# Kernel tuning notes

Measured on AMD Instinct MI355X. Metric: run time of the kernel, lower is better.

Reference implementation:

```python
import jax, jax.numpy as jnp
import numpy as np

BATCH, INPUT_DIM, BOND_DIM, OUTPUT_DIM = 4096, 1024, 32, 512


def setup_inputs() -> dict:
    key = jax.random.key(0)
    k1, k2, k3 = jax.random.split(key, 3)
    # inputs centered at 1 so the length-1024 chain product stays O(1) in fp32
    inputs = 1.0 + 0.05 * jax.random.normal(k1, (BATCH, INPUT_DIM), dtype=jnp.float32)
    # cores scaled ~ glorot so each [bond,bond] step roughly preserves norm
    cores = jax.random.normal(k2, (INPUT_DIM, BOND_DIM, BOND_DIM), dtype=jnp.float32) / jnp.sqrt(jnp.float32(BOND_DIM))
    projection = jax.random.normal(k3, (BOND_DIM, OUTPUT_DIM), dtype=jnp.float32) * 0.05
    bias = jnp.zeros((OUTPUT_DIM,), dtype=jnp.float32)
    return {"inputs": inputs, "cores": cores, "projection": projection, "bias": bias}


def reference(inputs, cores, projection, bias):
    # MPS chain: boundary_{i+1}[b,k] = sum_j boundary_i[b,j] * x_i[b] * core_i[j,k]
    batch = inputs.shape[0]
    bond = cores.shape[1]
    boundary0 = jnp.ones((batch, bond), dtype=inputs.dtype)

    def step(boundary, xc):
        x_i, core_i = xc  # x_i: [batch], core_i: [bond, bond]
        new_boundary = (boundary * x_i[:, None]) @ core_i  # [batch, bond]
        return new_boundary, None

    xs = (inputs.T, cores)  # scan over input_dim axis
    final_boundary, _ = jax.lax.scan(step, boundary0, xs)
    return final_boundary @ projection + bias
```

## Files before the change

kernel.cpp:

```cpp
#include <hip/hip_runtime.h>


__device__ __forceinline__ void mm32(const float* __restrict__ A,
                                     const float* __restrict__ B,
                                     float* __restrict__ C, int tid) {
    const int j = tid >> 3;
    const int kq = tid & 7;
    float a[32];
    const float4* __restrict__ A4 = (const float4*)(A + j * 32);
#pragma unroll
    for (int t = 0; t < 8; ++t) {
        float4 v = A4[t];
        a[4 * t + 0] = v.x; a[4 * t + 1] = v.y;
        a[4 * t + 2] = v.z; a[4 * t + 3] = v.w;
    }
    const float4* __restrict__ B4 = (const float4*)B;
    float4 acc = make_float4(0.f, 0.f, 0.f, 0.f);
#pragma unroll
    for (int m = 0; m < 32; ++m) {
        float4 b = B4[m * 8 + kq];
        acc.x = fmaf(a[m], b.x, acc.x);
        acc.y = fmaf(a[m], b.y, acc.y);
        acc.z = fmaf(a[m], b.z, acc.z);
        acc.w = fmaf(a[m], b.w, acc.w);
    }
    ((float4*)(C + j * 32))[kq] = acc;
}

__global__ __launch_bounds__(256) void k_seg4(const float* __restrict__ cores,
                                              float* __restrict__ l1) {
    __shared__ __align__(16) float c[4 * 1024];
    __shared__ __align__(16) float ping[1024];
    __shared__ __align__(16) float pong[1024];
    const int tid = threadIdx.x;
    const int s = blockIdx.x;
    const float4* src = (const float4*)(cores + (size_t)s * 4096);
    float4* cd = (float4*)c;
#pragma unroll
    for (int t = 0; t < 4; ++t) cd[tid + 256 * t] = src[tid + 256 * t];
    __syncthreads();
    mm32(c, c + 1024, ping, tid);
    __syncthreads();
    mm32(ping, c + 2048, pong, tid);
    __syncthreads();
    mm32(pong, c + 3072, ping, tid);
    __syncthreads();
    ((float4*)(l1 + (size_t)s * 1024))[tid] = ((const float4*)ping)[tid];
}

__global__ __launch_bounds__(256) void k_seg8(const float* __restrict__ l1,
                                              float* __restrict__ l2) {
    __shared__ __align__(16) float m[8 * 1024];
    __shared__ __align__(16) float ping[1024];
    __shared__ __align__(16) float pong[1024];
    const int tid = threadIdx.x;
    const int s = blockIdx.x;
    const float4* src = (const float4*)(l1 + (size_t)s * 8192);
    float4* md = (float4*)m;
#pragma unroll
    for (int t = 0; t < 8; ++t) md[tid + 256 * t] = src[tid + 256 * t];
    __syncthreads();
    mm32(m, m + 1024, ping, tid);
    __syncthreads();
    float* A = ping;
    float* C = pong;
    for (int t = 2; t < 8; ++t) {
        mm32(A, m + t * 1024, C, tid);
        __syncthreads();
        float* tmp = A; A = C; C = tmp;
    }
    ((float4*)(l2 + (size_t)s * 1024))[tid] = ((const float4*)A)[tid];
}

__global__ __launch_bounds__(64) void k_chain(const float* __restrict__ l2,
                                              const float* __restrict__ proj,
                                              float* __restrict__ q) {
    __shared__ __align__(16) float M[2][2048];
    __shared__ __align__(16) float sc[2][32];
    const int lane = threadIdx.x;
    const int k = lane & 31;
    const float4* src = (const float4*)l2;
    float4 pf[8];
#pragma unroll
    for (int t = 0; t < 8; ++t) pf[t] = src[lane + 64 * t];
#pragma unroll
    for (int t = 0; t < 8; ++t) ((float4*)M[0])[lane + 64 * t] = pf[t];
    __syncthreads();
    float v[32];
#pragma unroll
    for (int j = 0; j < 32; ++j) v[j] = 1.0f;
    for (int c = 0; c < 16; ++c) {
        if (c + 1 < 16) {
#pragma unroll
            for (int t = 0; t < 8; ++t)
                pf[t] = src[(c + 1) * 512 + lane + 64 * t];
        }
        const float* Mc = M[c & 1];
#pragma unroll
        for (int s = 0; s < 2; ++s) {
            const float* mat = Mc + s * 1024;
            float acc = 0.f;
#pragma unroll
            for (int j = 0; j < 32; ++j)
                acc = fmaf(v[j], mat[j * 32 + k], acc);
            const int pb = (2 * c + s) & 1;
            if (lane < 32) sc[pb][k] = acc;
            __syncthreads();
#pragma unroll
            for (int j = 0; j < 32; ++j) v[j] = sc[pb][j];
        }
        if (c + 1 < 16) {
            __syncthreads();
#pragma unroll
            for (int t = 0; t < 8; ++t)
                ((float4*)M[(c + 1) & 1])[lane + 64 * t] = pf[t];
            __syncthreads();
        }
    }
    const float4* P4 = (const float4*)proj;
    float4* q4 = (float4*)q;
#pragma unroll
    for (int h = 0; h < 2; ++h) {
        const int o4 = h * 64 + lane;
        float4 acc = make_float4(0.f, 0.f, 0.f, 0.f);
#pragma unroll
        for (int j = 0; j < 32; ++j) {
            float4 pv = P4[j * 128 + o4];
            acc.x = fmaf(v[j], pv.x, acc.x);
            acc.y = fmaf(v[j], pv.y, acc.y);
            acc.z = fmaf(v[j], pv.z, acc.z);
            acc.w = fmaf(v[j], pv.w, acc.w);
        }
        q4[o4] = acc;
    }
}

__global__ __launch_bounds__(256) void k_out(const float* __restrict__ inputs,
                                             const float* __restrict__ q,
                                             const float* __restrict__ bias,
                                             float* __restrict__ out) {
    const int lane = threadIdx.x & 63;
    const int wid = threadIdx.x >> 6;
    const int row = blockIdx.x * 4 + wid;
    const float4* in4 = (const float4*)(inputs + (size_t)row * 1024);
    float4 x0 = in4[lane];
    float4 x1 = in4[lane + 64];
    float4 x2 = in4[lane + 128];
    float4 x3 = in4[lane + 192];
    float p = ((x0.x * x0.y) * (x0.z * x0.w)) * ((x1.x * x1.y) * (x1.z * x1.w)) *
              ((x2.x * x2.y) * (x2.z * x2.w)) * ((x3.x * x3.y) * (x3.z * x3.w));
#pragma unroll
    for (int msk = 1; msk < 64; msk <<= 1) p *= __shfl_xor(p, msk);
    const float4* q4 = (const float4*)q;
    const float4* b4 = (const float4*)bias;
    float4* o4 = (float4*)(out + (size_t)row * 512);
#pragma unroll
    for (int t = 0; t < 2; ++t) {
        float4 qq = q4[lane + 64 * t];
        float4 bb = b4[lane + 64 * t];
        float4 r;
        r.x = fmaf(p, qq.x, bb.x);
        r.y = fmaf(p, qq.y, bb.y);
        r.z = fmaf(p, qq.z, bb.z);
        r.w = fmaf(p, qq.w, bb.w);
        o4[lane + 64 * t] = r;
    }
}

extern "C" void kernel_launch(void* const* d_in, const int* in_sizes, int n_in,
                              void* d_out, int out_size, void* d_ws, size_t ws_size,
                              hipStream_t stream) {
    const float* inputs = (const float*)d_in[0];
    const float* cores  = (const float*)d_in[1];
    const float* proj   = (const float*)d_in[2];
    const float* bias   = (const float*)d_in[3];
    float* out = (float*)d_out;
    float* w  = (float*)d_ws;
    float* l1 = w;
    float* l2 = w + 256 * 1024;
    float* q  = w + 256 * 1024 + 32 * 1024;

    k_seg4<<<256, 256, 0, stream>>>(cores, l1);
    k_seg8<<<32, 256, 0, stream>>>(l1, l2);
    k_chain<<<1, 64, 0, stream>>>(l2, proj, q);
    k_out<<<1024, 256, 0, stream>>>(inputs, q, bias, out);
}
```

Measured before the change: 101.0 us.

## Fuse row-product into core-segment kernel and rebalance chain reduction tree levels

Per-row input products are now computed in the first kernel, which loads the input rows while the 4-core segment products run, so the output kernel only reads a precomputed scalar. The second-level reduction now combines 16 segments per block (16 blocks) instead of 8, and the serial chain kernel handles 16 matrices using wave shuffles instead of LDS and barriers. The output kernel stages q and bias in LDS and writes 8 rows per block. The deeper second level does more serial matmuls per block with fewer blocks, trading parallelism for a shorter single-block serial tail.

```diff
diff --git a/kernel.cpp b/kernel.cpp
--- a/kernel.cpp
+++ b/kernel.cpp
@@ -27,17 +27,32 @@
     ((float4*)(C + j * 32))[kq] = acc;
 }
 
-__global__ __launch_bounds__(256) void k_seg4(const float* __restrict__ cores,
-                                              float* __restrict__ l1) {
+__global__ __launch_bounds__(256) void k1(const float* __restrict__ cores,
+                                          const float* __restrict__ inputs,
+                                          float* __restrict__ l1,
+                                          float* __restrict__ p) {
     __shared__ __align__(16) float c[4 * 1024];
     __shared__ __align__(16) float ping[1024];
     __shared__ __align__(16) float pong[1024];
     const int tid = threadIdx.x;
     const int s = blockIdx.x;
+    const int lane = tid & 63;
+    const int wid = tid >> 6;
+
     const float4* src = (const float4*)(cores + (size_t)s * 4096);
     float4* cd = (float4*)c;
 #pragma unroll
     for (int t = 0; t < 4; ++t) cd[tid + 256 * t] = src[tid + 256 * t];
+
+    float4 xr[16];
+#pragma unroll
+    for (int rr = 0; rr < 4; ++rr) {
+        const int row = s * 16 + wid * 4 + rr;
+        const float4* in4 = (const float4*)(inputs + (size_t)row * 1024);
+#pragma unroll
+        for (int t = 0; t < 4; ++t) xr[rr * 4 + t] = in4[lane + 64 * t];
+    }
+
     __syncthreads();
     mm32(c, c + 1024, ping, tid);
     __syncthreads();
@@ -46,25 +61,36 @@
     mm32(pong, c + 3072, ping, tid);
     __syncthreads();
     ((float4*)(l1 + (size_t)s * 1024))[tid] = ((const float4*)ping)[tid];
-}
-
-__global__ __launch_bounds__(256) void k_seg8(const float* __restrict__ l1,
-                                              float* __restrict__ l2) {
-    __shared__ __align__(16) float m[8 * 1024];
+
+#pragma unroll
+    for (int rr = 0; rr < 4; ++rr) {
+        float4 x0 = xr[rr * 4 + 0], x1 = xr[rr * 4 + 1];
+        float4 x2 = xr[rr * 4 + 2], x3 = xr[rr * 4 + 3];
+        float pr = ((x0.x * x0.y) * (x0.z * x0.w)) * ((x1.x * x1.y) * (x1.z * x1.w)) *
+                   ((x2.x * x2.y) * (x2.z * x2.w)) * ((x3.x * x3.y) * (x3.z * x3.w));
+#pragma unroll
+        for (int msk = 1; msk < 64; msk <<= 1) pr *= __shfl_xor(pr, msk);
+        if (lane == 0) p[s * 16 + wid * 4 + rr] = pr;
+    }
+}
+
+__global__ __launch_bounds__(256) void k2(const float* __restrict__ l1,
+                                          float* __restrict__ l2) {
+    __shared__ __align__(16) float m[16 * 1024];
     __shared__ __align__(16) float ping[1024];
     __shared__ __align__(16) float pong[1024];
     const int tid = threadIdx.x;
     const int s = blockIdx.x;
-    const float4* src = (const float4*)(l1 + (size_t)s * 8192);
+    const float4* src = (const float4*)(l1 + (size_t)s * 16384);
     float4* md = (float4*)m;
 #pragma unroll
-    for (int t = 0; t < 8; ++t) md[tid + 256 * t] = src[tid + 256 * t];
+    for (int t = 0; t < 16; ++t) md[tid + 256 * t] = src[tid + 256 * t];
     __syncthreads();
     mm32(m, m + 1024, ping, tid);
     __syncthreads();
     float* A = ping;
     float* C = pong;
-    for (int t = 2; t < 8; ++t) {
+    for (int t = 2; t < 16; ++t) {
         mm32(A, m + t * 1024, C, tid);
         __syncthreads();
         float* tmp = A; A = C; C = tmp;
@@ -72,98 +98,87 @@
     ((float4*)(l2 + (size_t)s * 1024))[tid] = ((const float4*)A)[tid];
 }
 
-__global__ __launch_bounds__(64) void k_chain(const float* __restrict__ l2,
-                                              const float* __restrict__ proj,
-                                              float* __restrict__ q) {
-    __shared__ __align__(16) float M[2][2048];
-    __shared__ __align__(16) float sc[2][32];
-    const int lane = threadIdx.x;
-    const int k = lane & 31;
+__global__ __launch_bounds__(256) void k3(const float* __restrict__ l2,
+                                          const float* __restrict__ proj,
+                                          float* __restrict__ q) {
+    __shared__ __align__(16) float M[16 * 1024];
+    __shared__ float w[32];
+    const int tid = threadIdx.x;
     const float4* src = (const float4*)l2;
-    float4 pf[8];
-#pragma unroll
-    for (int t = 0; t < 8; ++t) pf[t] = src[lane + 64 * t];
-#pragma unroll
-    for (int t = 0; t < 8; ++t) ((float4*)M[0])[lane + 64 * t] = pf[t];
-    __syncthreads();
-    float v[32];
-#pragma unroll
-    for (int j = 0; j < 32; ++j) v[j] = 1.0f;
-    for (int c = 0; c < 16; ++c) {
-        if (c + 1 < 16) {
-#pragma unroll
-            for (int t = 0; t < 8; ++t)
-                pf[t] = src[(c + 1) * 512 + lane + 64 * t];
+    float4* Md = (float4*)M;
+#pragma unroll
+    for (int t = 0; t < 16; ++t) Md[tid + 256 * t] = src[tid + 256 * t];
+    __syncthreads();
+
+    if (tid < 64) {
+        const int k = tid & 31;
+        const int h = tid >> 5;
+        float v[32];
+#pragma unroll
+        for (int j = 0; j < 32; ++j) v[j] = 1.0f;
+        for (int sm = 0; sm < 16; ++sm) {
+            const float* mat = M + sm * 1024;
+            float acc = 0.f;
+#pragma unroll
+            for (int j = 0; j < 16; ++j) {
+                const int jj = h * 16 + j;
+                acc = fmaf(v[jj], mat[jj * 32 + k], acc);
+            }
+            acc += __shfl_down(acc, 32);
+#pragma unroll
+            for (int j = 0; j < 32; ++j) v[j] = __shfl(acc, j);
         }
-        const float* Mc = M[c & 1];
-#pragma unroll
-        for (int s = 0; s < 2; ++s) {
-            const float* mat = Mc + s * 1024;
-            float acc = 0.f;
-#pragma unroll
-            for (int j = 0; j < 32; ++j)
-                acc = fmaf(v[j], mat[j * 32 + k], acc);
-            const int pb = (2 * c + s) & 1;
-            if (lane < 32) sc[pb][k] = acc;
-            __syncthreads();
-#pragma unroll
-            for (int j = 0; j < 32; ++j) v[j] = sc[pb][j];
+        if (tid < 32) w[k] = v[k];
+    }
+    __syncthreads();
+
+    if (tid < 128) {
+        const float4* P4 = (const float4*)proj;
+        float4 acc = make_float4(0.f, 0.f, 0.f, 0.f);
+#pragma unroll
+        for (int j = 0; j < 32; ++j) {
+            float wj = w[j];
+            float4 pv = P4[j * 128 + tid];
+            acc.x = fmaf(wj, pv.x, acc.x);
+            acc.y = fmaf(wj, pv.y, acc.y);
+            acc.z = fmaf(wj, pv.z, acc.z);
+            acc.w = fmaf(wj, pv.w, acc.w);
         }
-        if (c + 1 < 16) {
-            __syncthreads();
-#pragma unroll
-            for (int t = 0; t < 8; ++t)
-                ((float4*)M[(c + 1) & 1])[lane + 64 * t] = pf[t];
-            __syncthreads();
-        }
-    }
-    const float4* P4 = (const float4*)proj;
-    float4* q4 = (float4*)q;
-#pragma unroll
-    for (int h = 0; h < 2; ++h) {
-        const int o4 = h * 64 + lane;
-        float4 acc = make_float4(0.f, 0.f, 0.f, 0.f);
-#pragma unroll
-        for (int j = 0; j < 32; ++j) {
-            float4 pv = P4[j * 128 + o4];
-            acc.x = fmaf(v[j], pv.x, acc.x);
-            acc.y = fmaf(v[j], pv.y, acc.y);
-            acc.z = fmaf(v[j], pv.z, acc.z);
-            acc.w = fmaf(v[j], pv.w, acc.w);
-        }
-        q4[o4] = acc;
-    }
-}
-
-__global__ __launch_bounds__(256) void k_out(const float* __restrict__ inputs,
-                                             const float* __restrict__ q,
-                                             const float* __restrict__ bias,
-                                             float* __restrict__ out) {
-    const int lane = threadIdx.x & 63;
-    const int wid = threadIdx.x >> 6;
-    const int row = blockIdx.x * 4 + wid;
-    const float4* in4 = (const float4*)(inputs + (size_t)row * 1024);
-    float4 x0 = in4[lane];
-    float4 x1 = in4[lane + 64];
-    float4 x2 = in4[lane + 128];
-    float4 x3 = in4[lane + 192];
-    float p = ((x0.x * x0.y) * (x0.z * x0.w)) * ((x1.x * x1.y) * (x1.z * x1.w)) *
-              ((x2.x * x2.y) * (x2.z * x2.w)) * ((x3.x * x3.y) * (x3.z * x3.w));
-#pragma unroll
-    for (int msk = 1; msk < 64; msk <<= 1) p *= __shfl_xor(p, msk);
-    const float4* q4 = (const float4*)q;
-    const float4* b4 = (const float4*)bias;
+        ((float4*)q)[tid] = acc;
+    }
+}
+
+__global__ __launch_bounds__(256) void k4(const float* __restrict__ p,
+                                          const float* __restrict__ q,
+                                          const float* __restrict__ bias,
+                                          float* __restrict__ out) {
+    __shared__ __align__(16) float qL[512];
+    __shared__ __align__(16) float bL[512];
+    __shared__ float pL[8];
+    const int tid = threadIdx.x;
+    const int s = blockIdx.x;
+    if (tid < 128) {
+        ((float4*)qL)[tid] = ((const float4*)q)[tid];
+        ((float4*)bL)[tid] = ((const float4*)bias)[tid];
+    }
+    if (tid < 8) pL[tid] = p[s * 8 + tid];
+    __syncthreads();
+    const int row = s * 8 + (tid >> 5);
+    const float pr = pL[tid >> 5];
     float4* o4 = (float4*)(out + (size_t)row * 512);
-#pragma unroll
-    for (int t = 0; t < 2; ++t) {
-        float4 qq = q4[lane + 64 * t];
-        float4 bb = b4[lane + 64 * t];
+    const float4* q4 = (const float4*)qL;
+    const float4* b4 = (const float4*)bL;
+#pragma unroll
+    for (int u = 0; u < 4; ++u) {
+        const int c4 = u * 32 + (tid & 31);
+        float4 qq = q4[c4];
+        float4 bb = b4[c4];
         float4 r;
-        r.x = fmaf(p, qq.x, bb.x);
-        r.y = fmaf(p, qq.y, bb.y);
-        r.z = fmaf(p, qq.z, bb.z);
-        r.w = fmaf(p, qq.w, bb.w);
-        o4[lane + 64 * t] = r;
+        r.x = fmaf(pr, qq.x, bb.x);
+        r.y = fmaf(pr, qq.y, bb.y);
+        r.z = fmaf(pr, qq.z, bb.z);
+        r.w = fmaf(pr, qq.w, bb.w);
+        o4[c4] = r;
     }
 }
 
@@ -178,10 +193,11 @@
     float* w  = (float*)d_ws;
     float* l1 = w;
     float* l2 = w + 256 * 1024;
-    float* q  = w + 256 * 1024 + 32 * 1024;
-
-    k_seg4<<<256, 256, 0, stream>>>(cores, l1);
-    k_seg8<<<32, 256, 0, stream>>>(l1, l2);
-    k_chain<<<1, 64, 0, stream>>>(l2, proj, q);
-    k_out<<<1024, 256, 0, stream>>>(inputs, q, bias, out);
-}
+    float* q  = w + 256 * 1024 + 16 * 1024;
+    float* p  = w + 256 * 1024 + 16 * 1024 + 512;
+
+    k1<<<256, 256, 0, stream>>>(cores, inputs, l1, p);
+    k2<<<16, 256, 0, stream>>>(l1, l2);
+    k3<<<1, 256, 0, stream>>>(l2, proj, q);
+    k4<<<512, 256, 0, stream>>>(p, q, bias, out);
+}
```

Result: slower. 146.1 us (+44.6%).
